# Optimization experiments

Measured on AMD Instinct MI355X. Metric: run time of the kernel, lower is better.

The kernel has to match this reference:

```python
import jax, jax.numpy as jnp
import numpy as np


def setup_inputs() -> dict:
    key = jax.random.key(0)
    k1, k2 = jax.random.split(key)
    B, V = 256, 128000
    logits = jax.random.normal(k1, (B, V), dtype=jnp.float32)
    temperatures = jax.random.uniform(k2, (B,), dtype=jnp.float32, minval=0.0, maxval=1.5)
    # make a quarter of the sequences greedy (temperature == 0) to exercise both paths
    temperatures = temperatures.at[: B // 4].set(0.0)
    return {"logits": logits, "temperatures": temperatures}


def reference(logits, temperatures):
    # Temperature-scaled logits; temperature==0 rows use temp 1 for the (unused) sampling path.
    logits = logits.astype(jnp.float32)
    safe_t = jnp.where(temperatures == 0, jnp.ones_like(temperatures), temperatures)
    scaled = logits / safe_t[:, None]  # [B, V]

    # probs (same math as torch.softmax(scaled, -1)); materialized for faithfulness
    probs = jax.nn.softmax(scaled, axis=-1)

    greedy_tokens = jnp.argmax(logits, axis=-1)  # [B]

    # torch.multinomial(probs, 1) == Gumbel-max / categorical over scaled logits
    sample_key = jax.random.key(42)
    sampled_tokens = jax.random.categorical(sample_key, scaled, axis=-1)  # [B]

    return jnp.where(temperatures == 0, greedy_tokens, sampled_tokens)
```

## Files before the change

### kernel.cpp

```cpp
#include <hip/hip_runtime.h>
#include <stdint.h>

namespace {

constexpr int kB = 256;
constexpr int kV = 128000;
constexpr int kBlk = 256;
constexpr int kSubs = 5;
constexpr int kSpan = kV / kSubs;
constexpr int kF4 = 5;
constexpr int kTile = kBlk * 4 * kF4;
constexpr int kTiles = kSpan / kTile;

struct Part { float val; int idx; };

__device__ __forceinline__ uint32_t threefry_bits(uint32_t x1) {
  constexpr uint32_t ks0 = 0u;
  constexpr uint32_t ks1 = 42u;
  constexpr uint32_t ks2 = 0x1BD11BDAu ^ ks0 ^ ks1;
  uint32_t x0 = ks0;
  x1 += ks1;
#define TF_ROUND(r) { x0 += x1; x1 = __builtin_rotateleft32(x1, r); x1 ^= x0; }
  TF_ROUND(13) TF_ROUND(15) TF_ROUND(26) TF_ROUND(6)
  x0 += ks1; x1 += ks2 + 1u;
  TF_ROUND(17) TF_ROUND(29) TF_ROUND(16) TF_ROUND(24)
  x0 += ks2; x1 += ks0 + 2u;
  TF_ROUND(13) TF_ROUND(15) TF_ROUND(26) TF_ROUND(6)
  x0 += ks0; x1 += ks1 + 3u;
  TF_ROUND(17) TF_ROUND(29) TF_ROUND(16) TF_ROUND(24)
  x0 += ks1; x1 += ks2 + 4u;
  TF_ROUND(13) TF_ROUND(15) TF_ROUND(26) TF_ROUND(6)
  x0 += ks2; x1 += ks0 + 5u;
#undef TF_ROUND
  return x0 ^ x1;
}

__device__ __forceinline__ float gumbel_from_bits(uint32_t bits) {
  constexpr float kTiny = 1.17549435e-38f;
  constexpr float kNegLn2 = -0.69314718055994530942f;
  float f = __uint_as_float((bits >> 9) | 0x3F800000u) - 1.0f;
  float u = f + kTiny;
  float y = __builtin_amdgcn_logf(u) * kNegLn2;
  return __builtin_amdgcn_logf(y) * kNegLn2;
}

__global__ __launch_bounds__(kBlk) void sampler_partial(
    const float* __restrict__ logits, const float* __restrict__ temps,
    Part* __restrict__ parts) {
  const int r = blockIdx.x / kSubs;
  const int s = blockIdx.x % kSubs;
  const float t = temps[r];
  const float* __restrict__ row = logits + (size_t)r * kV + (size_t)s * kSpan;
  const int toff = (int)threadIdx.x * 4;

  float4 cur[kF4], nxt[kF4];

#define LOAD_TILE(dst, k)                                                     \
  {                                                                           \
    const float* g_ = row + (k) * kTile + toff;                               \
    _Pragma("unroll")                                                         \
    for (int i_ = 0; i_ < kF4; ++i_)                                          \
      dst[i_] = *reinterpret_cast<const float4*>(g_ + i_ * kBlk * 4);         \
  }

  float best = -__builtin_inff();
  int bi = 0;

  LOAD_TILE(cur, 0)

  if (t == 0.0f) {
#pragma unroll 1
    for (int k = 0; k < kTiles; ++k) {
      __builtin_amdgcn_sched_barrier(0);
      if (k + 1 < kTiles) LOAD_TILE(nxt, k + 1)
      __builtin_amdgcn_sched_barrier(0);
      const int ebase = s * kSpan + k * kTile + toff;
#pragma unroll
      for (int i = 0; i < kF4; ++i) {
        const int v = ebase + i * kBlk * 4;
        float la[4] = {cur[i].x, cur[i].y, cur[i].z, cur[i].w};
#pragma unroll
        for (int j = 0; j < 4; ++j) {
          if (la[j] > best) { best = la[j]; bi = v + j; }
        }
      }
      __builtin_amdgcn_sched_barrier(0);
#pragma unroll
      for (int i = 0; i < kF4; ++i) cur[i] = nxt[i];
    }
  } else {
#pragma unroll 1
    for (int k = 0; k < kTiles; ++k) {
      __builtin_amdgcn_sched_barrier(0);
      if (k + 1 < kTiles) LOAD_TILE(nxt, k + 1)
      __builtin_amdgcn_sched_barrier(0);
      const int ebase = s * kSpan + k * kTile + toff;
#pragma unroll
      for (int i = 0; i < kF4; ++i) {
        const int v = ebase + i * kBlk * 4;
        const uint32_t base = (uint32_t)(r * kV + v);
        float la[4] = {cur[i].x, cur[i].y, cur[i].z, cur[i].w};
#pragma unroll
        for (int j = 0; j < 4; ++j) {
          float gb = gumbel_from_bits(threefry_bits(base + (uint32_t)j));
          float key = fmaf(t, gb, la[j]);
          if (key > best) { best = key; bi = v + j; }
        }
      }
      __builtin_amdgcn_sched_barrier(0);
#pragma unroll
      for (int i = 0; i < kF4; ++i) cur[i] = nxt[i];
    }
  }
#undef LOAD_TILE

  __shared__ float sv[kBlk];
  __shared__ int si[kBlk];
  sv[threadIdx.x] = best;
  si[threadIdx.x] = bi;
  __syncthreads();
  for (int st = kBlk / 2; st > 0; st >>= 1) {
    if ((int)threadIdx.x < st) {
      float ov = sv[threadIdx.x + st]; int oi = si[threadIdx.x + st];
      float mv = sv[threadIdx.x];      int mi = si[threadIdx.x];
      if (ov > mv || (ov == mv && oi < mi)) {
        sv[threadIdx.x] = ov; si[threadIdx.x] = oi;
      }
    }
    __syncthreads();
  }
  if (threadIdx.x == 0) {
    parts[r * kSubs + s].val = sv[0];
    parts[r * kSubs + s].idx = si[0];
  }
}

__global__ __launch_bounds__(kB) void sampler_final(
    const Part* __restrict__ parts, int* __restrict__ out) {
  const int r = threadIdx.x;
  if (r < kB) {
    float bv = -__builtin_inff();
    int bi = 0;
#pragma unroll
    for (int g = 0; g < kSubs; ++g) {
      Part p = parts[r * kSubs + g];
      if (p.val > bv || (p.val == bv && p.idx < bi)) { bv = p.val; bi = p.idx; }
    }
    out[r] = bi;
  }
}

}

extern "C" void kernel_launch(void* const* d_in, const int* in_sizes, int n_in,
                              void* d_out, int out_size, void* d_ws, size_t ws_size,
                              hipStream_t stream) {
  const float* logits = (const float*)d_in[0];
  const float* temps = (const float*)d_in[1];
  int* out = (int*)d_out;
  Part* parts = (Part*)d_ws;

  sampler_partial<<<dim3(kB * kSubs), dim3(kBlk), 0, stream>>>(logits, temps, parts);
  sampler_final<<<dim3(1), dim3(kB), 0, stream>>>(parts, out);
}
```

Before: 209.9 us.

## Stage logits through LDS with async global_load_lds double buffering

After: 216.7 us. +3.3%, slower.

```diff
diff --git a/kernel.cpp b/kernel.cpp
--- a/kernel.cpp
+++ b/kernel.cpp
@@ -8,8 +8,7 @@
 constexpr int kBlk = 256;
 constexpr int kSubs = 5;
 constexpr int kSpan = kV / kSubs;
-constexpr int kF4 = 5;
-constexpr int kTile = kBlk * 4 * kF4;
+constexpr int kTile = kBlk * 4;
 constexpr int kTiles = kSpan / kTile;
 
 struct Part { float val; int idx; };
@@ -44,92 +43,88 @@
   return __builtin_amdgcn_logf(y) * kNegLn2;
 }
 
+typedef const __attribute__((address_space(1))) void* gas_ptr;
+typedef __attribute__((address_space(3))) void* las_ptr;
+
 __global__ __launch_bounds__(kBlk) void sampler_partial(
     const float* __restrict__ logits, const float* __restrict__ temps,
     Part* __restrict__ parts) {
   const int r = blockIdx.x / kSubs;
   const int s = blockIdx.x % kSubs;
+  const int tid = (int)threadIdx.x;
   const float t = temps[r];
-  const float* __restrict__ row = logits + (size_t)r * kV + (size_t)s * kSpan;
-  const int toff = (int)threadIdx.x * 4;
+  const float* __restrict__ seg = logits + (size_t)r * kV + (size_t)s * kSpan;
 
-  float4 cur[kF4], nxt[kF4];
+  __shared__ alignas(16) float stage_lds[2][kTile];
+  const int wavebase = (tid >> 6) << 8;
+  const float* gsrc = seg + tid * 4;
 
-#define LOAD_TILE(dst, k)                                                     \
-  {                                                                           \
-    const float* g_ = row + (k) * kTile + toff;                               \
-    _Pragma("unroll")                                                         \
-    for (int i_ = 0; i_ < kF4; ++i_)                                          \
-      dst[i_] = *reinterpret_cast<const float4*>(g_ + i_ * kBlk * 4);         \
-  }
+#define STAGE(b, k)                                                          \
+  __builtin_amdgcn_global_load_lds((gas_ptr)(gsrc + (k) * kTile),            \
+                                   (las_ptr)(&stage_lds[(b)][wavebase]),     \
+                                   16, 0, 0);
 
   float best = -__builtin_inff();
   int bi = 0;
 
-  LOAD_TILE(cur, 0)
+  STAGE(0, 0)
 
   if (t == 0.0f) {
 #pragma unroll 1
     for (int k = 0; k < kTiles; ++k) {
-      __builtin_amdgcn_sched_barrier(0);
-      if (k + 1 < kTiles) LOAD_TILE(nxt, k + 1)
-      __builtin_amdgcn_sched_barrier(0);
-      const int ebase = s * kSpan + k * kTile + toff;
-#pragma unroll
-      for (int i = 0; i < kF4; ++i) {
-        const int v = ebase + i * kBlk * 4;
-        float la[4] = {cur[i].x, cur[i].y, cur[i].z, cur[i].w};
-#pragma unroll
-        for (int j = 0; j < 4; ++j) {
-          if (la[j] > best) { best = la[j]; bi = v + j; }
-        }
+      if (k + 1 < kTiles) {
+        STAGE((k + 1) & 1, k + 1)
+        __builtin_amdgcn_s_waitcnt(0x0F71);
+      } else {
+        __builtin_amdgcn_s_waitcnt(0x0F70);
       }
       __builtin_amdgcn_sched_barrier(0);
+      float4 a = *reinterpret_cast<const float4*>(&stage_lds[k & 1][tid * 4]);
+      const int v = s * kSpan + k * kTile + tid * 4;
+      float la[4] = {a.x, a.y, a.z, a.w};
 #pragma unroll
-      for (int i = 0; i < kF4; ++i) cur[i] = nxt[i];
+      for (int j = 0; j < 4; ++j) {
+        if (la[j] > best) { best = la[j]; bi = v + j; }
+      }
     }
   } else {
 #pragma unroll 1
     for (int k = 0; k < kTiles; ++k) {
-      __builtin_amdgcn_sched_barrier(0);
-      if (k + 1 < kTiles) LOAD_TILE(nxt, k + 1)
-      __builtin_amdgcn_sched_barrier(0);
-      const int ebase = s * kSpan + k * kTile + toff;
-#pragma unroll
-      for (int i = 0; i < kF4; ++i) {
-        const int v = ebase + i * kBlk * 4;
-        const uint32_t base = (uint32_t)(r * kV + v);
-        float la[4] = {cur[i].x, cur[i].y, cur[i].z, cur[i].w};
-#pragma unroll
-        for (int j = 0; j < 4; ++j) {
-          float gb = gumbel_from_bits(threefry_bits(base + (uint32_t)j));
-          float key = fmaf(t, gb, la[j]);
-          if (key > best) { best = key; bi = v + j; }
-        }
+      if (k + 1 < kTiles) {
+        STAGE((k + 1) & 1, k + 1)
+        __builtin_amdgcn_s_waitcnt(0x0F71);
+      } else {
+        __builtin_amdgcn_s_waitcnt(0x0F70);
       }
       __builtin_amdgcn_sched_barrier(0);
+      float4 a = *reinterpret_cast<const float4*>(&stage_lds[k & 1][tid * 4]);
+      const int v = s * kSpan + k * kTile + tid * 4;
+      const uint32_t base = (uint32_t)(r * kV + v);
+      float la[4] = {a.x, a.y, a.z, a.w};
 #pragma unroll
-      for (int i = 0; i < kF4; ++i) cur[i] = nxt[i];
+      for (int j = 0; j < 4; ++j) {
+        float gb = gumbel_from_bits(threefry_bits(base + (uint32_t)j));
+        float key = fmaf(t, gb, la[j]);
+        if (key > best) { best = key; bi = v + j; }
+      }
     }
   }
-#undef LOAD_TILE
+#undef STAGE
 
   __shared__ float sv[kBlk];
   __shared__ int si[kBlk];
-  sv[threadIdx.x] = best;
-  si[threadIdx.x] = bi;
+  sv[tid] = best;
+  si[tid] = bi;
   __syncthreads();
   for (int st = kBlk / 2; st > 0; st >>= 1) {
-    if ((int)threadIdx.x < st) {
-      float ov = sv[threadIdx.x + st]; int oi = si[threadIdx.x + st];
-      float mv = sv[threadIdx.x];      int mi = si[threadIdx.x];
-      if (ov > mv || (ov == mv && oi < mi)) {
-        sv[threadIdx.x] = ov; si[threadIdx.x] = oi;
-      }
+    if (tid < st) {
+      float ov = sv[tid + st]; int oi = si[tid + st];
+      float mv = sv[tid];      int mi = si[tid];
+      if (ov > mv || (ov == mv && oi < mi)) { sv[tid] = ov; si[tid] = oi; }
     }
     __syncthreads();
   }
-  if (threadIdx.x == 0) {
+  if (tid == 0) {
     parts[r * kSubs + s].val = sv[0];
     parts[r * kSubs + s].idx = si[0];
   }
@@ -137,7 +132,7 @@
 
 __global__ __launch_bounds__(kB) void sampler_final(
     const Part* __restrict__ parts, int* __restrict__ out) {
-  const int r = threadIdx.x;
+  const int r = (int)threadIdx.x;
   if (r < kB) {
     float bv = -__builtin_inff();
     int bi = 0;
```
